# Performance work log

Hardware: AMD Instinct MI355X
Metric: run time of the kernel (lower is better)

The kernel has to match this reference:

```python
import jax, jax.numpy as jnp
import numpy as np

NQ = 10
C64 = jnp.complex64

# ---- gate matrices (built from traced fp32 params) ----

def u3(t, p, d):
    c = jnp.cos(t * 0.5).astype(C64)
    s = jnp.sin(t * 0.5).astype(C64)
    ep = jnp.exp(1j * p.astype(C64))
    ed = jnp.exp(1j * d.astype(C64))
    return jnp.stack([jnp.stack([c, -ed * s]), jnp.stack([ep * s, ep * ed * c])])

def ry(t):
    c = jnp.cos(t * 0.5).astype(C64)
    s = jnp.sin(t * 0.5).astype(C64)
    return jnp.stack([jnp.stack([c, -s]), jnp.stack([s, c])])

def rz(t):
    e = jnp.exp(-0.5j * t.astype(C64))
    ep = jnp.exp(0.5j * t.astype(C64))
    return jnp.diag(jnp.stack([e, ep]))

def rx(t):
    c = jnp.cos(t * 0.5).astype(C64)
    s = jnp.sin(t * 0.5).astype(C64)
    return jnp.stack([jnp.stack([c, -1j * s]), jnp.stack([-1j * s, c])])

def crz(t):
    one = jnp.ones((), C64)
    return jnp.diag(jnp.stack([one, one, jnp.exp(-0.5j * t.astype(C64)), jnp.exp(0.5j * t.astype(C64))]))

def crx(t):
    return jnp.eye(4, dtype=C64).at[2:, 2:].set(rx(t))

X = jnp.array([[0, 1], [1, 0]], dtype=C64)
CNOT = jnp.array([[1, 0, 0, 0], [0, 1, 0, 0], [0, 0, 0, 1], [0, 0, 1, 0]], dtype=C64)

# ---- gate application on state of shape (B, 2,...,2) ----

def ap1(st, U, w):
    ax = 1 + w
    s = jnp.moveaxis(st, ax, -1)
    s = s @ U.T
    return jnp.moveaxis(s, -1, ax)

def ap2(st, U, a, b):
    s = jnp.moveaxis(st, (1 + a, 1 + b), (-2, -1))
    sh = s.shape
    s = s.reshape(sh[:-2] + (4,)) @ U.T
    return jnp.moveaxis(s.reshape(sh), (-2, -1), (1 + a, 1 + b))

def conv_block(st, w, a, b):
    st = ap1(st, u3(w[0], w[1], w[2]), a)
    st = ap1(st, u3(w[3], w[4], w[5]), b)
    st = ap2(st, CNOT, a, b)
    st = ap1(st, ry(w[6]), a)
    st = ap1(st, rz(w[7]), b)
    st = ap2(st, CNOT, b, a)
    st = ap1(st, ry(w[8]), a)
    st = ap2(st, CNOT, a, b)
    st = ap1(st, u3(w[9], w[10], w[11]), a)
    st = ap1(st, u3(w[12], w[13], w[14]), b)
    return st

def pool_block(st, p, c, t):
    st = ap2(st, crz(p[0]), c, t)
    st = ap1(st, X, c)
    st = ap2(st, crx(p[1]), c, t)
    return st

def zexp(st, w):
    p = jnp.abs(st) ** 2  # fp32
    axes = tuple(ax for ax in range(1, NQ + 1) if ax != 1 + w)
    pz = p.sum(axis=axes)  # (B, 2)
    return pz[:, 0] - pz[:, 1]


def setup_inputs() -> dict:
    key = jax.random.key(0)
    ks = jax.random.split(key, 6)
    two_pi = 2.0 * np.pi
    return {
        "x": jax.random.normal(ks[0], (16384, 1024), dtype=jnp.float32),
        "weights_conv1": jax.random.uniform(ks[1], (10, 15), jnp.float32) * two_pi,
        "weights_conv2": jax.random.uniform(ks[2], (4, 15), jnp.float32) * two_pi,
        "weights_pool1": jax.random.uniform(ks[3], (5, 2), jnp.float32) * two_pi,
        "weights_pool2": jax.random.uniform(ks[4], (2, 2), jnp.float32) * two_pi,
        "weights_fc": jax.random.uniform(ks[5], (3,), jnp.float32) * two_pi,
    }


def reference(x, weights_conv1, weights_conv2, weights_pool1, weights_pool2, weights_fc):
    B = x.shape[0]
    # AmplitudeEmbedding with normalize=True (input already 1024-dim, no padding)
    nrm = jnp.linalg.norm(x, axis=1, keepdims=True)
    st = (x / nrm).astype(C64).reshape((B,) + (2,) * NQ)
    # conv layer 1: even pairs, odd pairs, wraparound (0, 9) reusing row 7
    for i in range(0, NQ, 2):
        st = conv_block(st, weights_conv1[i], i, i + 1)
    for i in range(1, NQ - 1, 2):
        st = conv_block(st, weights_conv1[i], i, i + 1)
    st = conv_block(st, weights_conv1[7], 0, NQ - 1)
    # pool layer 1
    for idx, i in enumerate(range(0, NQ, 2)):
        st = pool_block(st, weights_pool1[idx], i + 1, i)
    # conv layer 2 (stride-2 wires)
    for idx, i in enumerate(range(0, NQ - 2, 2)):
        st = conv_block(st, weights_conv2[idx], i, i + 2)
    # pool layer 2
    for idx, i in enumerate(range(0, NQ - 2, 4)):
        st = pool_block(st, weights_pool2[idx], i + 2, i)
    # fully-connected entanglers + RX rotations
    st = ap2(st, CNOT, 0, 4)
    st = ap2(st, CNOT, 2, 4)
    st = ap2(st, CNOT, 4, 0)
    st = ap1(st, rx(weights_fc[0]), 0)
    st = ap1(st, rx(weights_fc[1]), 2)
    st = ap1(st, rx(weights_fc[2]), 4)
    return jnp.stack([zexp(st, 0), zexp(st, 2)], axis=-1)  # (B, 2)
```

## Files before the change

### kernel.cpp

```cpp
#include <hip/hip_runtime.h>


typedef _Float16 f16;
typedef f16 f16x8 __attribute__((ext_vector_type(8)));
typedef f16 f16x4 __attribute__((ext_vector_type(4)));
typedef f16 f16x2 __attribute__((ext_vector_type(2)));
typedef float f32x4 __attribute__((ext_vector_type(4)));

__device__ inline float2 cmul(float2 a, float2 b) {
    return make_float2(a.x * b.x - a.y * b.y, a.x * b.y + a.y * b.x);
}
__device__ inline float2 cadd(float2 a, float2 b) {
    return make_float2(a.x + b.x, a.y + b.y);
}

struct M2 { float2 m[4]; };

__device__ inline M2 m2_u3(float t, float p, float d) {
    float c = cosf(0.5f * t), s = sinf(0.5f * t);
    float2 ep = make_float2(cosf(p), sinf(p));
    float2 ed = make_float2(cosf(d), sinf(d));
    M2 U;
    U.m[0] = make_float2(c, 0.f);
    U.m[1] = make_float2(-ed.x * s, -ed.y * s);
    U.m[2] = make_float2(ep.x * s, ep.y * s);
    float2 epd = cmul(ep, ed);
    U.m[3] = make_float2(epd.x * c, epd.y * c);
    return U;
}
__device__ inline M2 m2_ry(float t) {
    float c = cosf(0.5f * t), s = sinf(0.5f * t);
    M2 U;
    U.m[0] = make_float2(c, 0.f);  U.m[1] = make_float2(-s, 0.f);
    U.m[2] = make_float2(s, 0.f);  U.m[3] = make_float2(c, 0.f);
    return U;
}
__device__ inline M2 m2_rz(float t) {
    float c = cosf(0.5f * t), s = sinf(0.5f * t);
    M2 U;
    U.m[0] = make_float2(c, -s); U.m[1] = make_float2(0.f, 0.f);
    U.m[2] = make_float2(0.f, 0.f); U.m[3] = make_float2(c, s);
    return U;
}
__device__ inline M2 m2_rx(float t) {
    float c = cosf(0.5f * t), s = sinf(0.5f * t);
    M2 U;
    U.m[0] = make_float2(c, 0.f);   U.m[1] = make_float2(0.f, -s);
    U.m[2] = make_float2(0.f, -s);  U.m[3] = make_float2(c, 0.f);
    return U;
}

__device__ inline void ap2x2(float2& x, float2& y, const M2& U) {
    float2 nx = cadd(cmul(U.m[0], x), cmul(U.m[1], y));
    float2 ny = cadd(cmul(U.m[2], x), cmul(U.m[3], y));
    x = nx; y = ny;
}
__device__ inline void apA(float2 v[4], const M2& U) { ap2x2(v[0], v[2], U); ap2x2(v[1], v[3], U); }
__device__ inline void apB(float2 v[4], const M2& U) { ap2x2(v[0], v[1], U); ap2x2(v[2], v[3], U); }
__device__ inline void swapv(float2& a, float2& b) { float2 t = a; a = b; b = t; }

__device__ inline void conv_col(const float* w, float2 v[4]) {
    apA(v, m2_u3(w[0], w[1], w[2]));
    apB(v, m2_u3(w[3], w[4], w[5]));
    swapv(v[2], v[3]);
    apA(v, m2_ry(w[6]));
    apB(v, m2_rz(w[7]));
    swapv(v[1], v[3]);
    apA(v, m2_ry(w[8]));
    swapv(v[2], v[3]);
    apA(v, m2_u3(w[9], w[10], w[11]));
    apB(v, m2_u3(w[12], w[13], w[14]));
}
__device__ inline void pool_col(const float* p, float2 v[4]) {
    {
        float c = cosf(0.5f * p[0]), s = sinf(0.5f * p[0]);
        v[2] = cmul(v[2], make_float2(c, -s));
        v[3] = cmul(v[3], make_float2(c, s));
    }
    swapv(v[0], v[2]); swapv(v[1], v[3]);
    {
        M2 U = m2_rx(p[1]);
        ap2x2(v[2], v[3], U);
    }
}

__global__ void build_gates(const float* wc1, const float* wc2,
                            const float* wp1, const float* wp2,
                            const float* wfc, int2* gp, float2* gm) {
    const int t = threadIdx.x;
    const int n = t >> 2, c = t & 3;
    if (blockIdx.x != 0 || n >= 27) return;

    float2 v[4];
    for (int i = 0; i < 4; i++) v[i] = make_float2(0.f, 0.f);
    v[c] = make_float2(1.f, 0.f);

    int a, b;
    if (n < 5)        { int i = 2*n;       a = i;   b = i+1; conv_col(wc1 + 15*i, v); }
    else if (n < 9)   { int i = 2*(n-5)+1; a = i;   b = i+1; conv_col(wc1 + 15*i, v); }
    else if (n == 9)  { a = 0; b = 9;      conv_col(wc1 + 105, v); }
    else if (n < 15)  { int idx = n-10, i = 2*idx; a = i+1; b = i; pool_col(wp1 + 2*idx, v); }
    else if (n < 19)  { int idx = n-15, i = 2*idx; a = i; b = i+2; conv_col(wc2 + 15*idx, v); }
    else if (n == 19) { a = 2; b = 0;      pool_col(wp2 + 0, v); }
    else if (n == 20) { a = 6; b = 4;      pool_col(wp2 + 2, v); }
    else if (n <= 23) {
        a = (n == 21) ? 0 : (n == 22) ? 2 : 4;
        b = (n == 23) ? 0 : 4;
        swapv(v[2], v[3]);
    } else {
        a = (n == 24) ? 0 : (n == 25) ? 2 : 4;
        b = a + 1;
        apA(v, m2_rx(wfc[n - 24]));
    }
    if (c == 0) gp[n] = make_int2(9 - a, 9 - b);
    for (int i = 0; i < 4; i++) gm[n * 16 + i * 4 + c] = v[i];
}

#define SIM_BLOCKS 512
#define NORM_BLOCKS 2048

__global__ __launch_bounds__(256) void prep(const float* __restrict__ X,
                                            const int2* __restrict__ gp,
                                            const float2* __restrict__ gm,
                                            float* __restrict__ nrm2,
                                            f16* __restrict__ Xh,
                                            f16* __restrict__ BTh,
                                            float* __restrict__ out) {
    __shared__ float2 st[2][1025];
    const int bid = blockIdx.x;

    if (bid >= SIM_BLOCKS) {
        const int nb = bid - SIM_BLOCKS;
        const int w = threadIdx.x >> 6, l = threadIdx.x & 63;
        if (threadIdx.x < 16) out[nb * 16 + threadIdx.x] = 1.0f;
#pragma unroll
        for (int r = 0; r < 2; r++) {
            const int row = nb * 8 + w * 2 + r;
            const float4* xr = (const float4*)(X + (size_t)row * 1024);
            float s = 0.f;
#pragma unroll
            for (int ch = 0; ch < 4; ch++) {
                float4 v = xr[ch * 64 + l];
                f16x4 h;
                h[0] = (f16)v.x; h[1] = (f16)v.y; h[2] = (f16)v.z; h[3] = (f16)v.w;
                *(f16x4*)(Xh + (size_t)row * 1024 + (ch * 64 + l) * 4) = h;
                s += v.x * v.x + v.y * v.y + v.z * v.z + v.w * v.w;
            }
#pragma unroll
            for (int off = 32; off >= 1; off >>= 1) s += __shfl_xor(s, off, 64);
            if (l == 0) nrm2[row] = s;
        }
        return;
    }

    const int sb = bid;
    const int t0 = (sb & 7) * 128 + (sb >> 3) * 2;

    for (int i = threadIdx.x; i < 1024; i += 256) {
        st[0][i] = make_float2((i == t0) ? 1.f : 0.f, 0.f);
        st[1][i] = make_float2((i == t0 + 1) ? 1.f : 0.f, 0.f);
    }
    __syncthreads();

    for (int g = 0; g < 27; g++) {
        const int2 p = gp[g];
        float2 m[16];
#pragma unroll
        for (int i = 0; i < 16; i++) m[i] = gm[g * 16 + i];
        const int p1 = p.x, p2 = p.y;
        const int lo = min(p1, p2), hi = max(p1, p2);
        const int q = threadIdx.x;
        const int m1 = (1 << lo) - 1;
        int tt = (q & m1) | ((q & ~m1) << 1);
        const int m2m = (1 << hi) - 1;
        const int i0 = (tt & m2m) | ((tt & ~m2m) << 1);
        int idx[4];
        for (int ga = 0; ga < 2; ga++)
            for (int gb = 0; gb < 2; gb++)
                idx[2 * ga + gb] = i0 | (ga << p1) | (gb << p2);
#pragma unroll
        for (int c = 0; c < 2; c++) {
            float2 v[4];
#pragma unroll
            for (int i = 0; i < 4; i++) v[i] = st[c][idx[i]];
#pragma unroll
            for (int i = 0; i < 4; i++) {
                float2 s = make_float2(0.f, 0.f);
#pragma unroll
                for (int j = 0; j < 4; j++) s = cadd(s, cmul(m[i * 4 + j], v[j]));
                st[c][idx[i]] = s;
            }
        }
        __syncthreads();
    }

    for (int s = threadIdx.x; s < 1024; s += 256) {
        const int b9 = (s >> 9) & 1, b7 = (s >> 7) & 1;
        if (b9 | b7) {
            const int grp = b9 ? b7 : 2;
            const int pos = (((s >> 8) & 1) << 7) | (s & 127);
            const int np = grp * 256 + pos;
            f16x2 re, im;
#pragma unroll
            for (int c = 0; c < 2; c++) {
                re[c] = (f16)st[c][s].x;
                im[c] = (f16)st[c][s].y;
            }
            *(f16x2*)(BTh + (size_t)np * 1024 + t0) = re;
            *(f16x2*)(BTh + (size_t)(np + 768) * 1024 + t0) = im;
        }
    }
}

__device__ __forceinline__ void glds16(const void* g, void* l) {
    __builtin_amdgcn_global_load_lds(
        (const __attribute__((address_space(1))) void*)g,
        (__attribute__((address_space(3))) void*)l, 16, 0, 0);
}

__global__ __launch_bounds__(512, 2) void gemm_mfma(const f16* __restrict__ A,
                                                    const f16* __restrict__ Bt,
                                                    const float* __restrict__ nrm2,
                                                    float* __restrict__ out) {
    __shared__ char lds[131072];
    const int tid = threadIdx.x;
    const int l = tid & 63, w = tid >> 6;
    const int wr = w >> 1, wc = w & 1;
    const int row0 = blockIdx.x * 256, col0 = blockIdx.y * 128;

    const int srow = l >> 3;
    const int kc = (l & 7) ^ (srow & 7);
    const f16* aS = A  + (size_t)(row0 + 32 * w + srow) * 1024 + kc * 8;
    const f16* bS = Bt + (size_t)(col0 + 16 * w + srow) * 1024 + kc * 8;

    auto stageA = [&](int t, int p) {
        char* dst = lds + p * 32768 + (32 * w) * 128;
#pragma unroll
        for (int g = 0; g < 4; ++g)
            glds16(aS + t * 64 + g * 8 * 1024, dst + g * 1024);
    };
    auto stageB = [&](int t, int q) {
        char* dst = lds + 98304 + q * 16384 + (16 * w) * 128;
#pragma unroll
        for (int g = 0; g < 2; ++g)
            glds16(bS + t * 64 + g * 8 * 1024, dst + g * 1024);
    };

    int aOff[4][2], bOff[4][2];
#pragma unroll
    for (int i = 0; i < 4; i++)
#pragma unroll
        for (int h = 0; h < 2; h++) {
            const int cphys = (((l >> 4) + 4 * h) ^ (l & 7));
            aOff[i][h] = (wr * 64 + i * 16 + (l & 15)) * 128 + cphys * 16;
            bOff[i][h] = (wc * 64 + i * 16 + (l & 15)) * 128 + cphys * 16;
        }

    f32x4 acc[4][4];
    const f32x4 z = {0.f, 0.f, 0.f, 0.f};
#pragma unroll
    for (int i = 0; i < 4; i++)
#pragma unroll
        for (int j = 0; j < 4; j++) acc[i][j] = z;

    stageA(0, 0);
    stageB(0, 0);
    stageA(1, 1);
    asm volatile("s_waitcnt vmcnt(4)" ::: "memory");
    __builtin_amdgcn_s_barrier();
    __builtin_amdgcn_sched_barrier(0);

#pragma unroll
    for (int t = 0; t < 16; ++t) {
        const char* aB = lds + (t % 3) * 32768;
        const char* bB = lds + 98304 + (t & 1) * 16384;

        f16x8 af0[4], bf0[4];
#pragma unroll
        for (int i = 0; i < 4; i++) {
            af0[i] = *(const f16x8*)(aB + aOff[i][0]);
            bf0[i] = *(const f16x8*)(bB + bOff[i][0]);
        }
        if (t + 1 < 16) stageB(t + 1, (t + 1) & 1);
        if (t + 2 < 16) stageA(t + 2, (t + 2) % 3);
        __builtin_amdgcn_s_barrier();
        asm volatile("s_waitcnt lgkmcnt(0)" ::: "memory");
        __builtin_amdgcn_sched_barrier(0);
        __builtin_amdgcn_s_setprio(1);
#pragma unroll
        for (int mi = 0; mi < 4; mi++)
#pragma unroll
            for (int ni = 0; ni < 4; ni++)
                acc[mi][ni] = __builtin_amdgcn_mfma_f32_16x16x32_f16(
                    af0[mi], bf0[ni], acc[mi][ni], 0, 0, 0);
        __builtin_amdgcn_sched_barrier(0);
        __builtin_amdgcn_s_setprio(0);
        __builtin_amdgcn_s_barrier();

        f16x8 af1[4], bf1[4];
#pragma unroll
        for (int i = 0; i < 4; i++) {
            af1[i] = *(const f16x8*)(aB + aOff[i][1]);
            bf1[i] = *(const f16x8*)(bB + bOff[i][1]);
        }
        __builtin_amdgcn_s_barrier();
        asm volatile("s_waitcnt lgkmcnt(0)" ::: "memory");
        __builtin_amdgcn_sched_barrier(0);
        __builtin_amdgcn_s_setprio(1);
#pragma unroll
        for (int mi = 0; mi < 4; mi++)
#pragma unroll
            for (int ni = 0; ni < 4; ni++)
                acc[mi][ni] = __builtin_amdgcn_mfma_f32_16x16x32_f16(
                    af1[mi], bf1[ni], acc[mi][ni], 0, 0, 0);
        __builtin_amdgcn_sched_barrier(0);
        __builtin_amdgcn_s_setprio(0);
        if (t < 14) {
            asm volatile("s_waitcnt vmcnt(4)" ::: "memory");
        } else if (t == 14) {
            asm volatile("s_waitcnt vmcnt(0)" ::: "memory");
        }
        __builtin_amdgcn_s_barrier();
    }

    float c0[4][4], c1[4][4];
#pragma unroll
    for (int mi = 0; mi < 4; mi++)
#pragma unroll
        for (int rr = 0; rr < 4; rr++) { c0[mi][rr] = 0.f; c1[mi][rr] = 0.f; }
#pragma unroll
    for (int ni = 0; ni < 4; ni++) {
        const int n_glob = col0 + wc * 64 + ni * 16 + (l & 15);
        const int nm = (n_glob >= 768) ? n_glob - 768 : n_glob;
        const int grp = nm >> 8;
        const float w0 = (grp <= 1) ? 1.f : 0.f;
        const float w1 = (grp >= 1) ? 1.f : 0.f;
#pragma unroll
        for (int mi = 0; mi < 4; mi++)
#pragma unroll
            for (int rr = 0; rr < 4; rr++) {
                const float y = acc[mi][ni][rr];
                const float y2 = y * y;
                c0[mi][rr] += w0 * y2;
                c1[mi][rr] += w1 * y2;
            }
    }
#pragma unroll
    for (int off = 1; off < 16; off <<= 1)
#pragma unroll
        for (int mi = 0; mi < 4; mi++)
#pragma unroll
            for (int rr = 0; rr < 4; rr++) {
                c0[mi][rr] += __shfl_xor(c0[mi][rr], off, 64);
                c1[mi][rr] += __shfl_xor(c1[mi][rr], off, 64);
            }
    if ((l & 15) == 0) {
        const int q = l >> 4;
#pragma unroll
        for (int mi = 0; mi < 4; mi++)
#pragma unroll
            for (int rr = 0; rr < 4; rr++) {
                const int row = row0 + wr * 64 + mi * 16 + q * 4 + rr;
                const float inv = -2.0f / nrm2[row];
                atomicAdd(&out[row * 2 + 0], c0[mi][rr] * inv);
                atomicAdd(&out[row * 2 + 1], c1[mi][rr] * inv);
            }
    }
}

extern "C" void kernel_launch(void* const* d_in, const int* in_sizes, int n_in,
                              void* d_out, int out_size, void* d_ws, size_t ws_size,
                              hipStream_t stream) {
    const float* x   = (const float*)d_in[0];
    const float* wc1 = (const float*)d_in[1];
    const float* wc2 = (const float*)d_in[2];
    const float* wp1 = (const float*)d_in[3];
    const float* wp2 = (const float*)d_in[4];
    const float* wfc = (const float*)d_in[5];
    float* out = (float*)d_out;

    uintptr_t wsp = (uintptr_t)d_ws;
    int2*   gp     = (int2*)wsp;
    float2* gm     = (float2*)(wsp + 1024);
    f16*    BTh    = (f16*)(wsp + 8192);
    f16*    Xh     = (f16*)(wsp + 8192 + (3u << 20));
    float*  nrm2   = (float*)(wsp + 8192 + (35u << 20));

    build_gates<<<1, 128, 0, stream>>>(wc1, wc2, wp1, wp2, wfc, gp, gm);
    prep<<<SIM_BLOCKS + NORM_BLOCKS, 256, 0, stream>>>(x, gp, gm, nrm2, Xh, BTh, out);
    gemm_mfma<<<dim3(64, 12), 512, 0, stream>>>(Xh, BTh, nrm2, out);
}
```

Baseline: 217.2 us.

## Restructure GEMM mainloop pipeline, triple-buffer B, and remap tiles for XCD locality

The GEMM now triple-buffers B alongside A, issues the A and B loads together, and prefetches the first-half fragments of the next stage into registers. That cuts per-iteration barriers from three to one and removes the lgkmcnt waits and sched_barriers. The grid becomes 1D with a block-to-tile mapping that keeps row tiles on the same XCD, aiming for better L2 reuse of A. LDS grows to 144KB, so launch bounds drop to one block per CU, which lowers occupancy.

```diff
diff --git a/kernel.cpp b/kernel.cpp
--- a/kernel.cpp
+++ b/kernel.cpp
@@ -218,43 +218,49 @@
         (__attribute__((address_space(3))) void*)l, 16, 0, 0);
 }
 
-__global__ __launch_bounds__(512, 2) void gemm_mfma(const f16* __restrict__ A,
+__global__ __launch_bounds__(512, 1) void gemm_mfma(const f16* __restrict__ A,
                                                     const f16* __restrict__ Bt,
                                                     const float* __restrict__ nrm2,
                                                     float* __restrict__ out) {
-    __shared__ char lds[131072];
+    __shared__ char lds[147456];
     const int tid = threadIdx.x;
     const int l = tid & 63, w = tid >> 6;
     const int wr = w >> 1, wc = w & 1;
-    const int row0 = blockIdx.x * 256, col0 = blockIdx.y * 128;
+
+    const int lin = blockIdx.x;
+    const int xcd = lin & 7;
+    const int mm = lin >> 3;
+    const int rowT = xcd * 8 + mm / 12;
+    const int colT = mm % 12;
+    const int row0 = rowT * 256;
+    const int col0 = colT * 128;
 
     const int srow = l >> 3;
     const int kc = (l & 7) ^ (srow & 7);
     const f16* aS = A  + (size_t)(row0 + 32 * w + srow) * 1024 + kc * 8;
     const f16* bS = Bt + (size_t)(col0 + 16 * w + srow) * 1024 + kc * 8;
 
-    auto stageA = [&](int t, int p) {
-        char* dst = lds + p * 32768 + (32 * w) * 128;
+    auto stage = [&](int t, int p) {
+        char* aD = lds + p * 32768 + (32 * w) * 128;
+        char* bD = lds + 98304 + p * 16384 + (16 * w) * 128;
 #pragma unroll
         for (int g = 0; g < 4; ++g)
-            glds16(aS + t * 64 + g * 8 * 1024, dst + g * 1024);
+            glds16(aS + t * 64 + g * 8 * 1024, aD + g * 1024);
+#pragma unroll
+        for (int g = 0; g < 2; ++g)
+            glds16(bS + t * 64 + g * 8 * 1024, bD + g * 1024);
     };
-    auto stageB = [&](int t, int q) {
-        char* dst = lds + 98304 + q * 16384 + (16 * w) * 128;
-#pragma unroll
-        for (int g = 0; g < 2; ++g)
-            glds16(bS + t * 64 + g * 8 * 1024, dst + g * 1024);
-    };
 
     int aOff[4][2], bOff[4][2];
 #pragma unroll
-    for (int i = 0; i < 4; i++)
-#pragma unroll
-        for (int h = 0; h < 2; h++) {
-            const int cphys = (((l >> 4) + 4 * h) ^ (l & 7));
+    for (int h = 0; h < 2; h++) {
+        const int cphys = (((l >> 4) + 4 * h) ^ (l & 7));
+#pragma unroll
+        for (int i = 0; i < 4; i++) {
             aOff[i][h] = (wr * 64 + i * 16 + (l & 15)) * 128 + cphys * 16;
             bOff[i][h] = (wc * 64 + i * 16 + (l & 15)) * 128 + cphys * 16;
         }
+    }
 
     f32x4 acc[4][4];
     const f32x4 z = {0.f, 0.f, 0.f, 0.f};
@@ -263,64 +269,71 @@
 #pragma unroll
         for (int j = 0; j < 4; j++) acc[i][j] = z;
 
-    stageA(0, 0);
-    stageB(0, 0);
-    stageA(1, 1);
-    asm volatile("s_waitcnt vmcnt(4)" ::: "memory");
+    stage(0, 0);
+    stage(1, 1);
+    asm volatile("s_waitcnt vmcnt(6)" ::: "memory");
     __builtin_amdgcn_s_barrier();
-    __builtin_amdgcn_sched_barrier(0);
+    asm volatile("" ::: "memory");
+
+    f16x8 afA[4], bfA[4];
+    {
+        const char* aB = lds;
+        const char* bB = lds + 98304;
+#pragma unroll
+        for (int i = 0; i < 4; i++) {
+            afA[i] = *(const f16x8*)(aB + aOff[i][0]);
+            bfA[i] = *(const f16x8*)(bB + bOff[i][0]);
+        }
+    }
 
 #pragma unroll
     for (int t = 0; t < 16; ++t) {
         const char* aB = lds + (t % 3) * 32768;
-        const char* bB = lds + 98304 + (t & 1) * 16384;
-
-        f16x8 af0[4], bf0[4];
+        const char* bB = lds + 98304 + (t % 3) * 16384;
+
+        if (t + 2 < 16) stage(t + 2, (t + 2) % 3);
+
+        f16x8 afB[4], bfB[4];
 #pragma unroll
         for (int i = 0; i < 4; i++) {
-            af0[i] = *(const f16x8*)(aB + aOff[i][0]);
-            bf0[i] = *(const f16x8*)(bB + bOff[i][0]);
-        }
-        if (t + 1 < 16) stageB(t + 1, (t + 1) & 1);
-        if (t + 2 < 16) stageA(t + 2, (t + 2) % 3);
-        __builtin_amdgcn_s_barrier();
-        asm volatile("s_waitcnt lgkmcnt(0)" ::: "memory");
-        __builtin_amdgcn_sched_barrier(0);
+            afB[i] = *(const f16x8*)(aB + aOff[i][1]);
+            bfB[i] = *(const f16x8*)(bB + bOff[i][1]);
+        }
+
         __builtin_amdgcn_s_setprio(1);
 #pragma unroll
         for (int mi = 0; mi < 4; mi++)
 #pragma unroll
             for (int ni = 0; ni < 4; ni++)
                 acc[mi][ni] = __builtin_amdgcn_mfma_f32_16x16x32_f16(
-                    af0[mi], bf0[ni], acc[mi][ni], 0, 0, 0);
-        __builtin_amdgcn_sched_barrier(0);
+                    afA[mi], bfA[ni], acc[mi][ni], 0, 0, 0);
         __builtin_amdgcn_s_setprio(0);
-        __builtin_amdgcn_s_barrier();
-
-        f16x8 af1[4], bf1[4];
-#pragma unroll
-        for (int i = 0; i < 4; i++) {
-            af1[i] = *(const f16x8*)(aB + aOff[i][1]);
-            bf1[i] = *(const f16x8*)(bB + bOff[i][1]);
-        }
-        __builtin_amdgcn_s_barrier();
-        asm volatile("s_waitcnt lgkmcnt(0)" ::: "memory");
-        __builtin_amdgcn_sched_barrier(0);
+
         __builtin_amdgcn_s_setprio(1);
 #pragma unroll
         for (int mi = 0; mi < 4; mi++)
 #pragma unroll
             for (int ni = 0; ni < 4; ni++)
                 acc[mi][ni] = __builtin_amdgcn_mfma_f32_16x16x32_f16(
-                    af1[mi], bf1[ni], acc[mi][ni], 0, 0, 0);
-        __builtin_amdgcn_sched_barrier(0);
+                    afB[mi], bfB[ni], acc[mi][ni], 0, 0, 0);
         __builtin_amdgcn_s_setprio(0);
+
         if (t < 14) {
-            asm volatile("s_waitcnt vmcnt(4)" ::: "memory");
+            asm volatile("s_waitcnt vmcnt(6)" ::: "memory");
         } else if (t == 14) {
             asm volatile("s_waitcnt vmcnt(0)" ::: "memory");
         }
-        __builtin_amdgcn_s_barrier();
+        if (t < 15) {
+            __builtin_amdgcn_s_barrier();
+            asm volatile("" ::: "memory");
+            const char* aN = lds + ((t + 1) % 3) * 32768;
+            const char* bN = lds + 98304 + ((t + 1) % 3) * 16384;
+#pragma unroll
+            for (int i = 0; i < 4; i++) {
+                afA[i] = *(const f16x8*)(aN + aOff[i][0]);
+                bfA[i] = *(const f16x8*)(bN + bOff[i][0]);
+            }
+        }
     }
 
     float c0[4][4], c1[4][4];
@@ -355,12 +368,12 @@
                 c1[mi][rr] += __shfl_xor(c1[mi][rr], off, 64);
             }
     if ((l & 15) == 0) {
-        const int q = l >> 4;
+        const int q4 = l >> 4;
 #pragma unroll
         for (int mi = 0; mi < 4; mi++)
 #pragma unroll
             for (int rr = 0; rr < 4; rr++) {
-                const int row = row0 + wr * 64 + mi * 16 + q * 4 + rr;
+                const int row = row0 + wr * 64 + mi * 16 + q4 * 4 + rr;
                 const float inv = -2.0f / nrm2[row];
                 atomicAdd(&out[row * 2 + 0], c0[mi][rr] * inv);
                 atomicAdd(&out[row * 2 + 1], c1[mi][rr] * inv);
@@ -388,5 +401,5 @@
 
     build_gates<<<1, 128, 0, stream>>>(wc1, wc2, wp1, wp2, wfc, gp, gm);
     prep<<<SIM_BLOCKS + NORM_BLOCKS, 256, 0, stream>>>(x, gp, gm, nrm2, Xh, BTh, out);
-    gemm_mfma<<<dim3(64, 12), 512, 0, stream>>>(Xh, BTh, nrm2, out);
-}
+    gemm_mfma<<<768, 512, 0, stream>>>(Xh, BTh, nrm2, out);
+}
```

Measured after the change: 259.3 us. 1.19x slower.
